# Optimization experiments

Measured on AMD Instinct MI355X. Metric: run time of the kernel, lower is better.

The kernel has to match this reference:

```python
import jax, jax.numpy as jnp
import numpy as np

T, V, E, K, D, H, BERT = 4, 4096, 4096, 32, 8, 16, 768
CAT = H + BERT  # 784, second LSTM input size


def setup_inputs() -> dict:
    key = jax.random.key(0)
    ks = jax.random.split(key, 24)
    n = lambda k, s: jax.random.normal(k, s, dtype=jnp.float32) * 0.02
    return dict(
        prices=jax.random.normal(ks[0], (T, V, 1), dtype=jnp.float32),
        node_embs=jax.random.normal(ks[1], (T, E, BERT), dtype=jnp.float32),
        he_members=jax.random.randint(ks[2], (T, E, K), 0, V),
        vert_edges=jax.random.randint(ks[3], (T, V, D), 0, E),
        Wih_p=n(ks[4], (4 * H, 1)), Whh_p=n(ks[5], (4 * H, H)),
        bih_p=n(ks[6], (4 * H,)), bhh_p=n(ks[7], (4 * H,)),
        Wih_m=n(ks[8], (4 * H, CAT)), Whh_m=n(ks[9], (4 * H, H)),
        bih_m=n(ks[10], (4 * H,)), bhh_m=n(ks[11], (4 * H,)),
        vc_trans_w=n(ks[12], (K, K, H)), vc_trans_b=n(ks[13], (K, K)),
        vc_conv_w=n(ks[14], (K,)), vc_conv_b=n(ks[15], (1,)),
        ec_w1=n(ks[16], (CAT // 4, CAT)), ec_b1=n(ks[17], (CAT // 4,)),
        ec_w2=n(ks[18], (1, CAT // 4)), ec_b2=n(ks[19], (1,)),
        attn_in=n(ks[20], (H, H)), attn_out=n(ks[21], (H, 2 * H)),
        fc_w=n(ks[22], (2, H)), fc_b=n(ks[23], (2,)),
    )


def _lstm(x, Wih, Whh, bih, bhh):
    # x: (T, B, in) -> hidden states (T, B, H); PyTorch gate order i,f,g,o
    h0 = jnp.zeros((x.shape[1], Whh.shape[1]), x.dtype)
    b = bih + bhh

    def step(carry, xt):
        h, c = carry
        g = xt @ Wih.T + h @ Whh.T + b
        i, f, gg, o = jnp.split(g, 4, axis=-1)
        c = jax.nn.sigmoid(f) * c + jax.nn.sigmoid(i) * jnp.tanh(gg)
        h = jax.nn.sigmoid(o) * jnp.tanh(c)
        return (h, c), h

    _, hs = jax.lax.scan(step, (h0, h0), x)
    return hs


def reference(prices, node_embs, he_members, vert_edges,
              Wih_p, Whh_p, bih_p, bhh_p,
              Wih_m, Whh_m, bih_m, bhh_m,
              vc_trans_w, vc_trans_b, vc_conv_w, vc_conv_b,
              ec_w1, ec_b1, ec_w2, ec_b2,
              attn_in, attn_out, fc_w, fc_b):
    # price LSTM over lookback window: (T, V, 1) -> (T, V, H)
    new_prices = _lstm(prices, Wih_p, Whh_p, bih_p, bhh_p)

    # --- VertexConv (DHGNN): gather member price embeddings per hyperedge ---
    # reg[t,e,k] = new_prices[t, he_members[t,e,k]]  -> (T, E, K, H)
    reg = jax.vmap(lambda p, idx: p[idx])(new_prices, he_members)
    # grouped Conv1d(k, k*k, dim_in, groups=k): row i of multiplier depends on feat i
    mult = jnp.einsum('tekd,kjd->tekj', reg, vc_trans_w) + vc_trans_b
    mult = jax.nn.softmax(mult, axis=-1)                     # (T,E,K,K)
    trans = jnp.einsum('tekj,tejd->tekd', mult, reg)         # (T,E,K,H)
    he_emb = jnp.einsum('tekd,k->ted', trans, vc_conv_w) + vc_conv_b  # (T,E,H)

    # concat hyperedge emb with article embedding -> (T, E, 784)
    he_cat = jnp.concatenate([he_emb, node_embs], axis=-1)

    # --- EdgeConv: per-vertex attention over its D adjacent hyperedges ---
    ft = jax.vmap(lambda h, idx: h[idx])(he_cat, vert_edges)  # (T,V,D,CAT)
    s = jax.nn.relu(ft @ ec_w1.T + ec_b1) @ ec_w2.T + ec_b2   # (T,V,D,1)
    w = jax.nn.softmax(s, axis=2)
    hg = jnp.sum(w * ft, axis=2)                              # (T,V,CAT) == scatter into hg_tensor

    # second LSTM + residual with price embeddings
    lstm_out = _lstm(hg, Wih_m, Whh_m, bih_m, bhh_m)          # (T,V,H)
    la = lstm_out + new_prices

    # torchnlp 'general' Attention: query = last step, context = all steps
    q = la[-1] @ attn_in.T                                    # (V,H)
    ctx = jnp.transpose(la, (1, 0, 2))                        # (V,T,H)
    aw = jax.nn.softmax(jnp.einsum('vd,vtd->vt', q, ctx), axis=-1)
    mix = jnp.einsum('vt,vtd->vd', aw, ctx)
    attn = jnp.tanh(jnp.concatenate([mix, q], axis=-1) @ attn_out.T)  # (V,H)

    # final classifier (dropout identity in eval)
    return attn @ fc_w.T + fc_b                               # (V,2)
```

## Files before the change

### kernel.cpp

```cpp
#include <hip/hip_runtime.h>
#include <hip/hip_bf16.h>
#include <math.h>

#define TT 4
#define VV 4096
#define EE 4096
#define KK 32
#define DD 8
#define HH 16
#define BERTD 768
#define CATD 784
#define NH 196
#define NTOT 260
#define NSTEP 25
#define NPB 288

typedef __bf16 bf16x8 __attribute__((ext_vector_type(8)));
typedef float  f32x4  __attribute__((ext_vector_type(4)));

__device__ __forceinline__ float sigmoidf_(float x){ return 1.0f/(1.0f+expf(-x)); }
__device__ __forceinline__ unsigned short f2bf(float f){
  __bf16 h = (__bf16)f;
  return __builtin_bit_cast(unsigned short, h);
}
__device__ __forceinline__ float bf2f(unsigned short u){
  unsigned int x = ((unsigned int)u) << 16;
  return __builtin_bit_cast(float, x);
}
__device__ __forceinline__ uint4 pack8(float4 a, float4 b){
  uint4 u;
  u.x = (unsigned)f2bf(a.x) | ((unsigned)f2bf(a.y) << 16);
  u.y = (unsigned)f2bf(a.z) | ((unsigned)f2bf(a.w) << 16);
  u.z = (unsigned)f2bf(b.x) | ((unsigned)f2bf(b.y) << 16);
  u.w = (unsigned)f2bf(b.z) | ((unsigned)f2bf(b.w) << 16);
  return u;
}


__global__ __launch_bounds__(256) void kP(
    const float* __restrict__ prices,
    const float* __restrict__ Wih, const float* __restrict__ Whh,
    const float* __restrict__ bih, const float* __restrict__ bhh,
    float* __restrict__ np_out,
    const float* __restrict__ w1, const float* __restrict__ wm,
    unsigned short* __restrict__ Bbf,
    const float* __restrict__ tw, unsigned short* __restrict__ twbf,
    float* __restrict__ esc,
    const float* __restrict__ node, unsigned short* __restrict__ Abf){
  int b = blockIdx.x;
  int tid = threadIdx.x;
  if (b < 1024){
    int f16 = b;
    for (int i = tid; i < 1600; i += 256){
      int s = i >> 6, l = i & 63;
      int lr = l & 15, ls = l >> 4;
      int k = s*32 + ls*8;
      if (s == 0 && ls < 2) continue;
      uint4* dst = reinterpret_cast<uint4*>(&Abf[((size_t)(f16*NSTEP + s)*64 + l)*8]);
      if (k >= CATD){
        uint4 z = {0,0,0,0};
        *dst = z;
      } else {
        int row = f16*16 + lr;
        const float* src = &node[(size_t)row*BERTD + (k - 16)];
        float4 f0 = *reinterpret_cast<const float4*>(&src[0]);
        float4 f1 = *reinterpret_cast<const float4*>(&src[4]);
        *dst = pack8(f0, f1);
      }
    }
  } else if (b < 1280){
    int bb2 = b - 1024;
    int lane = tid & 15;
    int v    = (bb2*256 + tid) >> 4;
    float W[4][16], wih[4], bb[4];
#pragma unroll
    for (int gi=0; gi<4; ++gi){
      int j = gi*16 + lane;
      const float4* wr = reinterpret_cast<const float4*>(&Whh[j*16]);
      float4 w0=wr[0], w1v=wr[1], w2v=wr[2], w3v=wr[3];
      W[gi][0]=w0.x; W[gi][1]=w0.y; W[gi][2]=w0.z; W[gi][3]=w0.w;
      W[gi][4]=w1v.x; W[gi][5]=w1v.y; W[gi][6]=w1v.z; W[gi][7]=w1v.w;
      W[gi][8]=w2v.x; W[gi][9]=w2v.y; W[gi][10]=w2v.z; W[gi][11]=w2v.w;
      W[gi][12]=w3v.x; W[gi][13]=w3v.y; W[gi][14]=w3v.z; W[gi][15]=w3v.w;
      wih[gi] = Wih[j];
      bb[gi]  = bih[j] + bhh[j];
    }
    float h = 0.f, c = 0.f;
    for (int t=0; t<TT; ++t){
      float x = prices[t*VV + v];
      float a0 = fmaf(x, wih[0], bb[0]);
      float a1 = fmaf(x, wih[1], bb[1]);
      float a2 = fmaf(x, wih[2], bb[2]);
      float a3 = fmaf(x, wih[3], bb[3]);
#pragma unroll
      for (int d=0; d<16; ++d){
        float hb = __shfl(h, d, 16);
        a0 = fmaf(hb, W[0][d], a0);
        a1 = fmaf(hb, W[1][d], a1);
        a2 = fmaf(hb, W[2][d], a2);
        a3 = fmaf(hb, W[3][d], a3);
      }
      float ig = sigmoidf_(a0);
      float fg = sigmoidf_(a1);
      float gg = tanhf(a2);
      float og = sigmoidf_(a3);
      c = fmaf(fg, c, ig*gg);
      h = og * tanhf(c);
      np_out[(size_t)(t*VV+v)*16 + lane] = h;
    }
  } else if (b < 1298){
    int n16 = b - 1280;
    for (int i = tid; i < 1600; i += 256){
      int s = i >> 6, l = i & 63;
      int lr = l & 15, ls = l >> 4;
      int n = n16*16 + lr;
      int k = s*32 + ls*8;
      uint4* dst = reinterpret_cast<uint4*>(&Bbf[((size_t)(n16*NSTEP + s)*64 + l)*8]);
      if (n < NTOT && k < CATD){
        const float* src = (n < NH) ? &w1[(size_t)n*CATD + k]
                                    : &wm[(size_t)(n-NH)*CATD + k];
        float4 f0 = *reinterpret_cast<const float4*>(&src[0]);
        float4 f1 = *reinterpret_cast<const float4*>(&src[4]);
        *dst = pack8(f0, f1);
      } else {
        uint4 z = {0,0,0,0};
        *dst = z;
      }
    }
  } else if (b < 1300){
    int base = (b - 1298) * 512;
#pragma unroll
    for (int rr = 0; rr < 2; ++rr){
      int r = base + tid*2 + rr;
      const float* s = &tw[(size_t)r*16];
#pragma unroll
      for (int d = 0; d < 16; ++d) twbf[(size_t)r*16 + d] = f2bf(s[d]);
    }
  } else {
    int idx = ((b - 1300)*256 + tid)*4;
    float4 z = make_float4(0.f,0.f,0.f,0.f);
    *reinterpret_cast<float4*>(&esc[idx]) = z;
  }
}

__global__ __launch_bounds__(256) void k2_fused(
    const float* __restrict__ np, const int* __restrict__ mem,
    const unsigned short* __restrict__ twbf, const float* __restrict__ tb,
    const float* __restrict__ cw, const float* __restrict__ cb,
    unsigned short* __restrict__ Abf){
  __shared__ unsigned short s_reg[32*16*16];
  __shared__ float s_wsumP[4][16][32];
  __shared__ int   s_mem[512];
  int tid = threadIdx.x;
  int te0 = blockIdx.x * 16;
  for (int i = tid; i < 512; i += 256) s_mem[i] = mem[(size_t)te0*32 + i];
  __syncthreads();
  for (int p = tid; p < 512; p += 256){
    int gte = p & 15, gk = p >> 4;
    int t   = (te0 + gte) >> 12;
    int vid = s_mem[gte*32 + gk];
    const float4* src = reinterpret_cast<const float4*>(&np[((size_t)(t*VV) + vid)*16]);
    float4 f0 = src[0], f1 = src[1], f2 = src[2], f3 = src[3];
    uint4* dst = reinterpret_cast<uint4*>(&s_reg[(gk*16 + gte)*16]);
    dst[0] = pack8(f0, f1);
    dst[1] = pack8(f2, f3);
  }
  __syncthreads();
  int l = tid & 63;
  int w = tid >> 6;
  int lj = l & 15;
  int lg = l >> 4;
  float w0acc[4] = {0.f,0.f,0.f,0.f};
  float w1acc[4] = {0.f,0.f,0.f,0.f};
#pragma unroll
  for (int kk = 0; kk < 8; ++kk){
    int k = w*8 + kk;
    bf16x8 af = 0, b0 = 0, b1v = 0;
    if (l < 32){
      af  = *reinterpret_cast<const bf16x8*>(&s_reg[(k*16 + lj)*16 + lg*8]);
      b0  = *reinterpret_cast<const bf16x8*>(&twbf[((size_t)k*32 + lj)*16 + lg*8]);
      b1v = *reinterpret_cast<const bf16x8*>(&twbf[((size_t)k*32 + 16 + lj)*16 + lg*8]);
    }
    float tb0 = tb[k*32 + lj];
    float tb1 = tb[k*32 + 16 + lj];
    f32x4 c0 = {tb0, tb0, tb0, tb0};
    f32x4 c1 = {tb1, tb1, tb1, tb1};
    f32x4 s0 = __builtin_amdgcn_mfma_f32_16x16x32_bf16(af, b0,  c0, 0, 0, 0);
    f32x4 s1 = __builtin_amdgcn_mfma_f32_16x16x32_bf16(af, b1v, c1, 0, 0, 0);
    float cwk = cw[k];
#pragma unroll
    for (int i = 0; i < 4; ++i){
      float v0 = s0[i], v1 = s1[i];
      float m = fmaxf(v0, v1);
#pragma unroll
      for (int off = 1; off < 16; off <<= 1) m = fmaxf(m, __shfl_xor(m, off, 16));
      float e0 = expf(v0 - m), e1 = expf(v1 - m);
      float sm = e0 + e1;
#pragma unroll
      for (int off = 1; off < 16; off <<= 1) sm += __shfl_xor(sm, off, 16);
      float f = cwk / sm;
      w0acc[i] = fmaf(e0, f, w0acc[i]);
      w1acc[i] = fmaf(e1, f, w1acc[i]);
    }
  }
#pragma unroll
  for (int i = 0; i < 4; ++i){
    int ter = lg*4 + i;
    s_wsumP[w][ter][lj]      = w0acc[i];
    s_wsumP[w][ter][16 + lj] = w1acc[i];
  }
  __syncthreads();
  int te = tid >> 4, d = tid & 15;
  float he = cb[0];
#pragma unroll
  for (int j = 0; j < 32; ++j){
    float ws = s_wsumP[0][te][j] + s_wsumP[1][te][j]
             + s_wsumP[2][te][j] + s_wsumP[3][te][j];
    he = fmaf(ws, bf2f(s_reg[(j*16 + te)*16 + d]), he);
  }
  int f16 = blockIdx.x;
  Abf[((size_t)(f16*NSTEP + 0)*64 + (d >> 3)*16 + te)*8 + (d & 7)] = f2bf(he);
}

__global__ __launch_bounds__(256) void k3_gemm_mfma(
    const unsigned short* __restrict__ Abf,
    const unsigned short* __restrict__ Bbf, const float* __restrict__ b1,
    const float* __restrict__ w2, float* __restrict__ esc,
    float* __restrict__ C_pe){
  __shared__ unsigned short Bs[3*NSTEP*64*8];
  int tid = threadIdx.x;
  int bid = blockIdx.x;
  int group = bid / 48;
  int within = bid - group*48;
  int nc  = within >> 3;
  int mbr = within & 7;
  int mb  = group*8 + mbr;
  {
    const uint4* src = reinterpret_cast<const uint4*>(&Bbf[(size_t)(nc*3)*NSTEP*64*8]);
    uint4* dst = reinterpret_cast<uint4*>(Bs);
    for (int i = tid; i < 4800; i += 256) dst[i] = src[i];
  }
  __syncthreads();
  int l = tid & 63, w = tid >> 6;
  int lr = l & 15, ls = l >> 4;
  int m0 = mb*128 + w*32;
  int f16 = (m0 >> 4);
  const unsigned short* a0p = &Abf[(size_t)f16*NSTEP*512];
  f32x4 acc[2][3] = {};
#pragma unroll
  for (int s = 0; s < NSTEP; ++s){
    bf16x8 af0 = *reinterpret_cast<const bf16x8*>(&a0p[(s*64 + l)*8]);
    bf16x8 af1 = *reinterpret_cast<const bf16x8*>(&a0p[((NSTEP + s)*64 + l)*8]);
#pragma unroll
    for (int j = 0; j < 3; ++j){
      bf16x8 bfv = *reinterpret_cast<const bf16x8*>(&Bs[((j*NSTEP + s)*64 + l)*8]);
      acc[0][j] = __builtin_amdgcn_mfma_f32_16x16x32_bf16(af0, bfv, acc[0][j], 0, 0, 0);
      acc[1][j] = __builtin_amdgcn_mfma_f32_16x16x32_bf16(af1, bfv, acc[1][j], 0, 0, 0);
    }
  }
  float p[2][4] = {{0.f,0.f,0.f,0.f},{0.f,0.f,0.f,0.f}};
#pragma unroll
  for (int j = 0; j < 3; ++j){
    int n = nc*48 + j*16 + lr;
    bool hid = (n < NH);
    float b1n = hid ? b1[n] : 0.f;
    float w2n = hid ? w2[n] : 0.f;
#pragma unroll
    for (int i = 0; i < 2; ++i){
#pragma unroll
      for (int q = 0; q < 4; ++q){
        float v = acc[i][j][q];
        if (hid){
          p[i][q] += fmaxf(v + b1n, 0.f) * w2n;
        } else if (n < NTOT){
          int m = m0 + i*16 + ls*4 + q;
          C_pe[(size_t)m*64 + (n - NH)] = v;
        }
      }
    }
  }
  if (nc*48 < NH){
#pragma unroll
    for (int i = 0; i < 2; ++i){
#pragma unroll
      for (int q = 0; q < 4; ++q){
        float v = p[i][q];
#pragma unroll
        for (int off = 1; off < 16; off <<= 1) v += __shfl_xor(v, off, 16);
        if (lr == 0){
          int m = m0 + i*16 + ls*4 + q;
          atomicAdd(&esc[m], v);
        }
      }
    }
  }
}

__global__ __launch_bounds__(256) void k456(
    const int* __restrict__ ve, const float* __restrict__ esc,
    const float* __restrict__ C_pe, const float* __restrict__ np,
    const float* __restrict__ Whh, const float* __restrict__ bih,
    const float* __restrict__ bhh,
    const float* __restrict__ ain, const float* __restrict__ aout,
    const float* __restrict__ fcw, const float* __restrict__ fcb,
    float* __restrict__ out){
  __shared__ float s_ain[16*17];
  __shared__ float s_aout[16*33];
  __shared__ float s_fc[32];
  __shared__ float s_fcb[2];
  int tid = threadIdx.x;
  { int j = tid >> 4, d = tid & 15; s_ain[j*17+d] = ain[tid]; }
  for (int i = tid; i < 512; i += 256){ int j = i >> 5, d = i & 31; s_aout[j*33+d] = aout[i]; }
  if (tid < 32) s_fc[tid] = fcw[tid];
  if (tid < 2)  s_fcb[tid] = fcb[tid];
  int lane = tid & 15;
  int v = (blockIdx.x*256 + tid) >> 4;
  float W[4][16], b[4];
#pragma unroll
  for (int gi=0; gi<4; ++gi){
    int j = gi*16 + lane;
    const float4* wr = reinterpret_cast<const float4*>(&Whh[j*16]);
    float4 w0=wr[0], w1=wr[1], w2=wr[2], w3=wr[3];
    W[gi][0]=w0.x; W[gi][1]=w0.y; W[gi][2]=w0.z; W[gi][3]=w0.w;
    W[gi][4]=w1.x; W[gi][5]=w1.y; W[gi][6]=w1.z; W[gi][7]=w1.w;
    W[gi][8]=w2.x; W[gi][9]=w2.y; W[gi][10]=w2.z; W[gi][11]=w2.w;
    W[gi][12]=w3.x; W[gi][13]=w3.y; W[gi][14]=w3.z; W[gi][15]=w3.w;
    b[gi] = bih[j] + bhh[j];
  }
  __syncthreads();
  float h = 0.f, c = 0.f;
  float la0, la1, la2, la3;
#pragma unroll
  for (int t=0; t<TT; ++t){
    const int* vp = &ve[((size_t)(t*VV) + v)*8];
    int e[8]; float wv[8];
    float mx = -1e30f;
#pragma unroll
    for (int d = 0; d < 8; ++d){
      e[d] = vp[d];
      wv[d] = esc[(t << 12) + e[d]];
      mx = fmaxf(mx, wv[d]);
    }
    float s = 0.f;
#pragma unroll
    for (int d = 0; d < 8; ++d){ wv[d] = expf(wv[d]-mx); s += wv[d]; }
    float inv = 1.f/s;
#pragma unroll
    for (int d = 0; d < 8; ++d) wv[d] *= inv;
    float g0 = b[0], g1 = b[1], g2 = b[2], g3 = b[3];
#pragma unroll
    for (int d = 0; d < 8; ++d){
      const float* cp = &C_pe[(size_t)((t << 12) + e[d])*64];
      g0 = fmaf(wv[d], cp[lane],      g0);
      g1 = fmaf(wv[d], cp[16 + lane], g1);
      g2 = fmaf(wv[d], cp[32 + lane], g2);
      g3 = fmaf(wv[d], cp[48 + lane], g3);
    }
#pragma unroll
    for (int d=0; d<16; ++d){
      float hb = __shfl(h, d, 16);
      g0 = fmaf(hb, W[0][d], g0);
      g1 = fmaf(hb, W[1][d], g1);
      g2 = fmaf(hb, W[2][d], g2);
      g3 = fmaf(hb, W[3][d], g3);
    }
    float ig = sigmoidf_(g0);
    float fg = sigmoidf_(g1);
    float gg = tanhf(g2);
    float og = sigmoidf_(g3);
    c = fmaf(fg, c, ig*gg);
    h = og * tanhf(c);
    float la = h + np[(size_t)(t*VV+v)*16 + lane];
    if (t == 0) la0 = la; else if (t == 1) la1 = la;
    else if (t == 2) la2 = la; else la3 = la;
  }
  float q = 0.f;
#pragma unroll
  for (int d=0; d<16; ++d){
    float bb = __shfl(la3, d, 16);
    q = fmaf(bb, s_ain[lane*17+d], q);
  }
  float aw0 = q*la0, aw1 = q*la1, aw2 = q*la2, aw3 = q*la3;
#pragma unroll
  for (int off=1; off<16; off<<=1){
    aw0 += __shfl_xor(aw0, off, 16);
    aw1 += __shfl_xor(aw1, off, 16);
    aw2 += __shfl_xor(aw2, off, 16);
    aw3 += __shfl_xor(aw3, off, 16);
  }
  float mx = fmaxf(fmaxf(aw0,aw1), fmaxf(aw2,aw3));
  aw0 = expf(aw0-mx); aw1 = expf(aw1-mx); aw2 = expf(aw2-mx); aw3 = expf(aw3-mx);
  float inv = 1.f/(aw0+aw1+aw2+aw3);
  float mix = (aw0*la0 + aw1*la1 + aw2*la2 + aw3*la3) * inv;
  float a = 0.f;
#pragma unroll
  for (int d=0; d<16; ++d){
    float m  = __shfl(mix, d, 16);
    float qq = __shfl(q,  d, 16);
    a = fmaf(m,  s_aout[lane*33+d],    a);
    a = fmaf(qq, s_aout[lane*33+16+d], a);
  }
  float at = tanhf(a);
  float p0 = at * s_fc[lane];
  float p1 = at * s_fc[16+lane];
#pragma unroll
  for (int off=1; off<16; off<<=1){
    p0 += __shfl_xor(p0, off, 16);
    p1 += __shfl_xor(p1, off, 16);
  }
  if (lane == 0){
    out[(size_t)v*2 + 0] = p0 + s_fcb[0];
    out[(size_t)v*2 + 1] = p1 + s_fcb[1];
  }
}

extern "C" void kernel_launch(void* const* d_in, const int* in_sizes, int n_in,
                              void* d_out, int out_size, void* d_ws, size_t ws_size,
                              hipStream_t stream){
  const float* prices = (const float*)d_in[0];
  const float* node   = (const float*)d_in[1];
  const int*   mem    = (const int*)d_in[2];
  const int*   ve     = (const int*)d_in[3];
  const float* Wih_p  = (const float*)d_in[4];
  const float* Whh_p  = (const float*)d_in[5];
  const float* bih_p  = (const float*)d_in[6];
  const float* bhh_p  = (const float*)d_in[7];
  const float* Wih_m  = (const float*)d_in[8];
  const float* Whh_m  = (const float*)d_in[9];
  const float* bih_m  = (const float*)d_in[10];
  const float* bhh_m  = (const float*)d_in[11];
  const float* tw     = (const float*)d_in[12];
  const float* tb     = (const float*)d_in[13];
  const float* cw     = (const float*)d_in[14];
  const float* cb     = (const float*)d_in[15];
  const float* w1     = (const float*)d_in[16];
  const float* b1     = (const float*)d_in[17];
  const float* w2     = (const float*)d_in[18];
  const float* ain    = (const float*)d_in[20];
  const float* aout   = (const float*)d_in[21];
  const float* fcw    = (const float*)d_in[22];
  const float* fcb    = (const float*)d_in[23];

  float* np_buf = (float*)d_ws;
  float* esc    = np_buf + (size_t)TT*VV*HH;
  float* C_pe   = esc    + (size_t)TT*EE;
  unsigned short* Bbf  = (unsigned short*)(C_pe + (size_t)TT*EE*64);
  unsigned short* twbf = Bbf + (size_t)18*NSTEP*512;
  unsigned short* Abf  = twbf + (size_t)1024*16;

  kP<<<1316, 256, 0, stream>>>(prices, Wih_p, Whh_p, bih_p, bhh_p, np_buf,
                               w1, Wih_m, Bbf, tw, twbf, esc, node, Abf);
  k2_fused<<<(TT*EE)/16, 256, 0, stream>>>(np_buf, mem, twbf, tb, cw, cb, Abf);
  k3_gemm_mfma<<<768, 256, 0, stream>>>(Abf, Bbf, b1, w2, esc, C_pe);
  k456<<<(VV*16)/256, 256, 0, stream>>>(ve, esc, C_pe, np_buf, Whh_m, bih_m, bhh_m,
                                        ain, aout, fcw, fcb, (float*)d_out);
}
```

Baseline: 206.0 us.

## Drop LDS staging of B in GEMM and split vertex gather across two half-groups

The MFMA GEMM kernel now reads B fragments straight from global memory instead of first copying a B slab into shared memory and synchronizing. This removes the LDS fill and barrier but relies on the cache to serve B reuse across waves. The final LSTM/attention kernel now uses 32 threads per vertex, with each 16-lane half handling 4 of the 8 adjacent hyperedges. Softmax max and sum and the gate partials are combined with cross-half shuffles, which doubles the thread count to expose more parallelism in the latency-bound gather. The recurrent part is computed redundantly in both halves, and only one lane writes the output.

```diff
diff --git a/kernel.cpp b/kernel.cpp
--- a/kernel.cpp
+++ b/kernel.cpp
@@ -227,7 +227,6 @@
     const unsigned short* __restrict__ Bbf, const float* __restrict__ b1,
     const float* __restrict__ w2, float* __restrict__ esc,
     float* __restrict__ C_pe){
-  __shared__ unsigned short Bs[3*NSTEP*64*8];
   int tid = threadIdx.x;
   int bid = blockIdx.x;
   int group = bid / 48;
@@ -235,17 +234,12 @@
   int nc  = within >> 3;
   int mbr = within & 7;
   int mb  = group*8 + mbr;
-  {
-    const uint4* src = reinterpret_cast<const uint4*>(&Bbf[(size_t)(nc*3)*NSTEP*64*8]);
-    uint4* dst = reinterpret_cast<uint4*>(Bs);
-    for (int i = tid; i < 4800; i += 256) dst[i] = src[i];
-  }
-  __syncthreads();
   int l = tid & 63, w = tid >> 6;
   int lr = l & 15, ls = l >> 4;
   int m0 = mb*128 + w*32;
   int f16 = (m0 >> 4);
   const unsigned short* a0p = &Abf[(size_t)f16*NSTEP*512];
+  const unsigned short* bp  = &Bbf[(size_t)(nc*3)*NSTEP*512];
   f32x4 acc[2][3] = {};
 #pragma unroll
   for (int s = 0; s < NSTEP; ++s){
@@ -253,7 +247,7 @@
     bf16x8 af1 = *reinterpret_cast<const bf16x8*>(&a0p[((NSTEP + s)*64 + l)*8]);
 #pragma unroll
     for (int j = 0; j < 3; ++j){
-      bf16x8 bfv = *reinterpret_cast<const bf16x8*>(&Bs[((j*NSTEP + s)*64 + l)*8]);
+      bf16x8 bfv = *reinterpret_cast<const bf16x8*>(&bp[((size_t)(j*NSTEP + s)*64 + l)*8]);
       acc[0][j] = __builtin_amdgcn_mfma_f32_16x16x32_bf16(af0, bfv, acc[0][j], 0, 0, 0);
       acc[1][j] = __builtin_amdgcn_mfma_f32_16x16x32_bf16(af1, bfv, acc[1][j], 0, 0, 0);
     }
@@ -314,7 +308,8 @@
   if (tid < 32) s_fc[tid] = fcw[tid];
   if (tid < 2)  s_fcb[tid] = fcb[tid];
   int lane = tid & 15;
-  int v = (blockIdx.x*256 + tid) >> 4;
+  int half = (tid >> 4) & 1;
+  int v = (blockIdx.x*256 + tid) >> 5;
   float W[4][16], b[4];
 #pragma unroll
   for (int gi=0; gi<4; ++gi){
@@ -328,34 +323,48 @@
     b[gi] = bih[j] + bhh[j];
   }
   __syncthreads();
-  float h = 0.f, c = 0.f;
-  float la0, la1, la2, la3;
+  float g[4][4];
 #pragma unroll
   for (int t=0; t<TT; ++t){
-    const int* vp = &ve[((size_t)(t*VV) + v)*8];
-    int e[8]; float wv[8];
+    const int* vp = &ve[((size_t)(t*VV) + v)*8 + half*4];
+    int e[4]; float wv[4];
     float mx = -1e30f;
 #pragma unroll
-    for (int d = 0; d < 8; ++d){
+    for (int d = 0; d < 4; ++d){
       e[d] = vp[d];
       wv[d] = esc[(t << 12) + e[d]];
       mx = fmaxf(mx, wv[d]);
     }
+    mx = fmaxf(mx, __shfl_xor(mx, 16, 32));
     float s = 0.f;
 #pragma unroll
-    for (int d = 0; d < 8; ++d){ wv[d] = expf(wv[d]-mx); s += wv[d]; }
+    for (int d = 0; d < 4; ++d){ wv[d] = expf(wv[d]-mx); s += wv[d]; }
+    s += __shfl_xor(s, 16, 32);
     float inv = 1.f/s;
-#pragma unroll
-    for (int d = 0; d < 8; ++d) wv[d] *= inv;
-    float g0 = b[0], g1 = b[1], g2 = b[2], g3 = b[3];
-#pragma unroll
-    for (int d = 0; d < 8; ++d){
+    float g0 = 0.f, g1 = 0.f, g2 = 0.f, g3 = 0.f;
+#pragma unroll
+    for (int d = 0; d < 4; ++d){
       const float* cp = &C_pe[(size_t)((t << 12) + e[d])*64];
       g0 = fmaf(wv[d], cp[lane],      g0);
       g1 = fmaf(wv[d], cp[16 + lane], g1);
       g2 = fmaf(wv[d], cp[32 + lane], g2);
       g3 = fmaf(wv[d], cp[48 + lane], g3);
     }
+    g[t][0] = g0*inv; g[t][1] = g1*inv; g[t][2] = g2*inv; g[t][3] = g3*inv;
+  }
+#pragma unroll
+  for (int t=0; t<TT; ++t)
+#pragma unroll
+    for (int gi=0; gi<4; ++gi)
+      g[t][gi] += __shfl_xor(g[t][gi], 16, 32);
+  float h = 0.f, c = 0.f;
+  float la0, la1, la2, la3;
+#pragma unroll
+  for (int t=0; t<TT; ++t){
+    float g0 = g[t][0] + b[0];
+    float g1 = g[t][1] + b[1];
+    float g2 = g[t][2] + b[2];
+    float g3 = g[t][3] + b[3];
 #pragma unroll
     for (int d=0; d<16; ++d){
       float hb = __shfl(h, d, 16);
@@ -408,7 +417,7 @@
     p0 += __shfl_xor(p0, off, 16);
     p1 += __shfl_xor(p1, off, 16);
   }
-  if (lane == 0){
+  if ((tid & 31) == 0){
     out[(size_t)v*2 + 0] = p0 + s_fcb[0];
     out[(size_t)v*2 + 1] = p1 + s_fcb[1];
   }
@@ -452,6 +461,6 @@
                                w1, Wih_m, Bbf, tw, twbf, esc, node, Abf);
   k2_fused<<<(TT*EE)/16, 256, 0, stream>>>(np_buf, mem, twbf, tb, cw, cb, Abf);
   k3_gemm_mfma<<<768, 256, 0, stream>>>(Abf, Bbf, b1, w2, esc, C_pe);
-  k456<<<(VV*16)/256, 256, 0, stream>>>(ve, esc, C_pe, np_buf, Whh_m, bih_m, bhh_m,
+  k456<<<(VV*32)/256, 256, 0, stream>>>(ve, esc, C_pe, np_buf, Whh_m, bih_m, bhh_m,
                                         ain, aout, fcw, fcb, (float*)d_out);
 }
```

Result: faster. 197.2 us (-4.3%).
